# Kernel tuning notes

Hardware: AMD Instinct MI355X
Metric: run time of the kernel (lower is better)

Reference implementation:

```python
import jax, jax.numpy as jnp
import numpy as np

H = 1024

def gru_step(x, h, W_ih, W_hh, b_ih, b_hh):
    # torch.nn.GRUCell math; gate order r, z, n
    gi = x @ W_ih.T + b_ih            # [N, 3H]
    gh = h @ W_hh.T + b_hh            # [N, 3H]
    i_r, i_z, i_n = jnp.split(gi, 3, axis=-1)
    h_r, h_z, h_n = jnp.split(gh, 3, axis=-1)
    r = jax.nn.sigmoid(i_r + h_r)
    z = jax.nn.sigmoid(i_z + h_z)
    n = jnp.tanh(i_n + r * h_n)
    return (1.0 - z) * n + z * h


def setup_inputs() -> dict:
    key = jax.random.key(0)
    ks = jax.random.split(key, 12)
    V, Nr, Na = 256, 4096, 4096
    s = 1.0 / np.sqrt(H)
    return {
        'state': jax.random.normal(ks[0], (1, H), jnp.float32),
        'rel_tokens': jax.random.randint(ks[1], (Nr, 3), 0, V, jnp.int32),
        'attr_tokens': jax.random.randint(ks[2], (Na, 2), 0, V, jnp.int32),
        'table': jax.random.normal(ks[3], (V, H), jnp.float32),
        'W_emb': jax.random.normal(ks[4], (H, H), jnp.float32) * s,
        'b_emb': jnp.zeros((H,), jnp.float32),
        'W_ih': jax.random.normal(ks[5], (3 * H, H), jnp.float32) * s,
        'W_hh': jax.random.normal(ks[6], (3 * H, H), jnp.float32) * s,
        'b_ih': jnp.zeros((3 * H,), jnp.float32),
        'b_hh': jnp.zeros((3 * H,), jnp.float32),
        'W1': jax.random.normal(ks[7], (H, H), jnp.float32) * s,
        'b1': jnp.zeros((H,), jnp.float32),
        'W2': jax.random.normal(ks[8], (H, H), jnp.float32) * s,
        'b2': jnp.zeros((H,), jnp.float32),
        'W3': jax.random.normal(ks[9], (1, H), jnp.float32) * s,
        'b3': jnp.zeros((1,), jnp.float32),
        'eps': jax.random.uniform(ks[10], (1,), jnp.float32) * 0.1,
    }


def reference(state, rel_tokens, attr_tokens, table, W_emb, b_emb,
              W_ih, W_hh, b_ih, b_hh, W1, b1, W2, b2, W3, b3, eps):
    Nr, Na = rel_tokens.shape[0], attr_tokens.shape[0]
    # per-clause token embeddings passed through embedding_layer (Linear)
    rel_e = jnp.einsum('nte,he->nth', table[rel_tokens], W_emb) + b_emb   # [Nr,3,H]
    att_e = jnp.einsum('nte,he->nth', table[attr_tokens], W_emb) + b_emb  # [Na,2,H]

    # relation clauses: 3 chained GRU steps from global state
    h = jnp.broadcast_to(state, (Nr, H))
    for t in range(3):
        h = gru_step(rel_e[:, t], h, W_ih, W_hh, b_ih, b_hh)
    rel_h = h
    # attribute clauses: 2 chained GRU steps from global state
    h = jnp.broadcast_to(state, (Na, H))
    for t in range(2):
        h = gru_step(att_e[:, t], h, W_ih, W_hh, b_ih, b_hh)
    attr_h = h

    clause = jnp.concatenate([rel_h, attr_h], axis=0)          # [N, H]
    x = jax.nn.relu(clause @ W1.T + b1)
    x = jax.nn.relu(x @ W2.T + b2)
    logits = (x @ W3.T + b3).reshape(1, -1)                    # [1, N]
    probs = jax.nn.softmax(logits, axis=1)                     # softmax over clauses
    n = jnp.float32(probs.shape[1])
    probs = probs * (1.0 - eps[0]) + eps[0] / n                # eps smoothing
    return probs
```

## Files before the change

kernel.cpp:

```cpp
#include <hip/hip_runtime.h>
#include <math.h>

#define H 1024
#define H3 3072
#define NVOC 256

typedef __attribute__((ext_vector_type(8))) short bf16x8;
typedef __attribute__((ext_vector_type(4))) float f32x4;

__device__ __forceinline__ float sigf(float x) { return 1.0f / (1.0f + expf(-x)); }

__device__ __forceinline__ unsigned short f2bf(float f) {
    unsigned int u = __float_as_uint(f);
    u = (u + 0x7fffu + ((u >> 16) & 1u)) >> 16;
    return (unsigned short)u;
}
__device__ __forceinline__ float bf2f(unsigned short u) {
    return __uint_as_float(((unsigned int)u) << 16);
}

#define MM256(MH, AV, BV)                                                          \
    __builtin_amdgcn_s_setprio(1);                                                 \
    _Pragma("unroll")                                                              \
    for (int m_ = 0; m_ < 4; ++m_)                                                 \
        _Pragma("unroll")                                                          \
        for (int n_ = 0; n_ < 4; ++n_)                                             \
            acc[(MH) * 4 + m_][n_] = __builtin_amdgcn_mfma_f32_16x16x32_bf16(      \
                AV[m_], BV[n_], acc[(MH) * 4 + m_][n_], 0, 0, 0);                  \
    __builtin_amdgcn_s_setprio(0);

#define RDA256(BUF, MH, KQ)                                                        \
    _Pragma("unroll")                                                              \
    for (int m_ = 0; m_ < 4; ++m_)                                                 \
        a[m_] = *reinterpret_cast<const bf16x8*>(                                  \
            ldsb + (BUF) * 65536 + (g * 128 + (MH) * 64 + m_ * 16 + fr) * 128 +    \
            (((KQ) * 4 + fq) ^ (fr & 7)) * 16);

#define RDB256(BUF, KQ, DST)                                                       \
    _Pragma("unroll")                                                              \
    for (int n_ = 0; n_ < 4; ++n_)                                                 \
        DST[n_] = *reinterpret_cast<const bf16x8*>(                                \
            ldsb + (BUF) * 65536 + 32768 + (wn + n_ * 16 + fr) * 128 +             \
            (((KQ) * 4 + fq) ^ (fr & 7)) * 16);

#define BAR256() __builtin_amdgcn_s_barrier()

template<bool RELU, int OUT_MODE>
__global__ __launch_bounds__(512, 2)
void gemm256(const unsigned short* __restrict__ A, const unsigned short* __restrict__ W,
             const float* __restrict__ bias, void* __restrict__ C,
             int N, int K, int gx,
             const float* __restrict__ w3, float* __restrict__ logits)
{
    __shared__ unsigned short lds[65536];
    char* ldsb = (char*)lds;
    const int tid = threadIdx.x;
    const int wid = tid >> 6, lane = tid & 63;

    const int nwg = gridDim.x;
    const int cpx = nwg >> 3;
    const int bid = blockIdx.x;
    const int swz = (bid & 7) * cpx + (bid >> 3);
    const int bm = (swz / gx) * 256;
    const int bn = (swz % gx) * 256;

    const int g = wid >> 2;
    const int wn = (wid & 3) * 64;
    const int fr = lane & 15, fq = lane >> 4;

    const int sr = tid >> 3;
    const int sc = ((tid & 7) ^ (sr & 7)) * 8;
    auto stage_unit = [&](int t, int u) {
        const unsigned short* src = (u < 4)
            ? A + (size_t)(bm + u * 64 + sr) * K + t * 64 + sc
            : W + (size_t)(bn + (u - 4) * 64 + sr) * K + t * 64 + sc;
        char* dst = ldsb + (t & 1) * 65536 + u * 8192 + tid * 16;
        __builtin_amdgcn_global_load_lds(
            (const __attribute__((address_space(1))) void*)src,
            (__attribute__((address_space(3))) void*)dst, 16, 0, 0);
    };

    f32x4 acc[8][4];
#pragma unroll
    for (int i = 0; i < 8; i++)
#pragma unroll
        for (int j = 0; j < 4; j++) acc[i][j] = (f32x4){0.f, 0.f, 0.f, 0.f};
    bf16x8 a[4], b0[4], b1[4];

    const int nt = K >> 6;

#pragma unroll
    for (int u = 0; u < 8; ++u) stage_unit(0, u);
    stage_unit(1, 0); stage_unit(1, 2); stage_unit(1, 4);
    stage_unit(1, 5); stage_unit(1, 6); stage_unit(1, 7);
    asm volatile("s_waitcnt vmcnt(6)" ::: "memory");
    __builtin_amdgcn_sched_barrier(0);
    BAR256();

    for (int t = 0; t < nt; ++t) {
        const int buf = t & 1;
        RDB256(buf, 0, b0); RDA256(buf, 0, 0);
        if (t + 1 < nt) stage_unit(t + 1, 1);
        MM256(0, a, b0); BAR256();
        RDB256(buf, 1, b1); RDA256(buf, 0, 1);
        if (t + 1 < nt) stage_unit(t + 1, 3);
        MM256(0, a, b1); BAR256();
        RDA256(buf, 1, 0);
        if (t + 2 < nt) { stage_unit(t + 2, 0); stage_unit(t + 2, 2); stage_unit(t + 2, 4); }
        MM256(1, a, b0); BAR256();
        RDA256(buf, 1, 1);
        if (t + 2 < nt) { stage_unit(t + 2, 5); stage_unit(t + 2, 6); stage_unit(t + 2, 7); }
        MM256(1, a, b1);
        if (t + 2 < nt) {
            asm volatile("s_waitcnt vmcnt(6)" ::: "memory");
            __builtin_amdgcn_sched_barrier(0);
        } else if (t + 1 < nt) {
            asm volatile("s_waitcnt vmcnt(0)" ::: "memory");
            __builtin_amdgcn_sched_barrier(0);
        }
        BAR256();
    }

    if (OUT_MODE == 2) {
        float rs[8][4];
#pragma unroll
        for (int m = 0; m < 8; m++)
#pragma unroll
            for (int j = 0; j < 4; j++) rs[m][j] = 0.f;
#pragma unroll
        for (int n = 0; n < 4; n++) {
            const int col = bn + wn + n * 16 + fr;
            const float bv = bias[col];
            const float wv = w3[col];
#pragma unroll
            for (int m = 0; m < 8; m++)
#pragma unroll
                for (int j = 0; j < 4; j++) {
                    float v = acc[m][n][j] + bv;
                    if (RELU) v = fmaxf(v, 0.f);
                    rs[m][j] = fmaf(v, wv, rs[m][j]);
                }
        }
#pragma unroll
        for (int m = 0; m < 8; m++)
#pragma unroll
            for (int j = 0; j < 4; j++) {
                float s = rs[m][j];
                s += __shfl_xor(s, 1); s += __shfl_xor(s, 2);
                s += __shfl_xor(s, 4); s += __shfl_xor(s, 8);
                if (fr == 0) {
                    const int row = bm + g * 128 + (m >> 2) * 64 + (m & 3) * 16 + fq * 4 + j;
                    atomicAdd(logits + row, s);
                }
            }
    } else {
#pragma unroll
        for (int m = 0; m < 8; m++) {
#pragma unroll
            for (int n = 0; n < 4; n++) {
                const int col = bn + wn + n * 16 + fr;
                const float bv = bias[col];
#pragma unroll
                for (int j = 0; j < 4; j++) {
                    const int row = bm + g * 128 + (m >> 2) * 64 + (m & 3) * 16 + fq * 4 + j;
                    float v = acc[m][n][j] + bv;
                    if (RELU) v = fmaxf(v, 0.f);
                    ((unsigned short*)C)[(size_t)row * N + col] = f2bf(v);
                }
            }
        }
    }
}

template<bool RELU, int OUT_MODE>
__global__ __launch_bounds__(512, 2)
void gemm_n(const unsigned short* __restrict__ A, const unsigned short* __restrict__ W,
            const float* __restrict__ bias, void* __restrict__ C,
            int N, int K, int gx,
            const float* __restrict__ w3, float* __restrict__ logits)
{
    __shared__ unsigned short lds[73728];
    char* ldsb = (char*)lds;
    const int tid = threadIdx.x;
    const int wid = tid >> 6, lane = tid & 63;

    const int nwg = gridDim.x;
    const int cpx = nwg >> 3;
    const int bid = blockIdx.x;
    const int swz = (bid & 7) * cpx + (bid >> 3);
    const int bm = (swz / gx) * 128;
    const int bn = (swz % gx) * 256;

    const int g = wid >> 2;
    const int wn = (wid & 3) * 64;
    const int fr = lane & 15, fq = lane >> 4;

    const int sr = tid >> 3;
    const int sc = ((tid & 7) ^ (sr & 7)) * 8;
    auto stage_unit = [&](int t, int u) {
        const unsigned short* src = (u < 2)
            ? A + (size_t)(bm + u * 64 + sr) * K + t * 64 + sc
            : W + (size_t)(bn + (u - 2) * 64 + sr) * K + t * 64 + sc;
        char* dst = ldsb + (t % 3) * 49152 + u * 8192 + tid * 16;
        __builtin_amdgcn_global_load_lds(
            (const __attribute__((address_space(1))) void*)src,
            (__attribute__((address_space(3))) void*)dst, 16, 0, 0);
    };

    f32x4 acc[4][4];
#pragma unroll
    for (int i = 0; i < 4; i++)
#pragma unroll
        for (int j = 0; j < 4; j++) acc[i][j] = (f32x4){0.f, 0.f, 0.f, 0.f};
    bf16x8 a[4], b[4];

    const int nt = K >> 6;

#pragma unroll
    for (int u = 0; u < 6; ++u) stage_unit(0, u);
#pragma unroll
    for (int u = 0; u < 6; ++u) stage_unit(1, u);
    asm volatile("s_waitcnt vmcnt(6)" ::: "memory");
    __builtin_amdgcn_sched_barrier(0);
    __builtin_amdgcn_s_barrier();

    for (int t = 0; t < nt; ++t) {
        const int buf = (t % 3) * 49152;
#pragma unroll
        for (int n_ = 0; n_ < 4; ++n_)
            b[n_] = *reinterpret_cast<const bf16x8*>(
                ldsb + buf + 16384 + (wn + n_ * 16 + fr) * 128 + ((fq) ^ (fr & 7)) * 16);
#pragma unroll
        for (int m_ = 0; m_ < 4; ++m_)
            a[m_] = *reinterpret_cast<const bf16x8*>(
                ldsb + buf + (g * 64 + m_ * 16 + fr) * 128 + ((fq) ^ (fr & 7)) * 16);
        if (t + 2 < nt) { stage_unit(t + 2, 0); stage_unit(t + 2, 1); stage_unit(t + 2, 2); }
        __builtin_amdgcn_s_setprio(1);
#pragma unroll
        for (int m_ = 0; m_ < 4; ++m_)
#pragma unroll
            for (int n_ = 0; n_ < 4; ++n_)
                acc[m_][n_] = __builtin_amdgcn_mfma_f32_16x16x32_bf16(a[m_], b[n_], acc[m_][n_], 0, 0, 0);
        __builtin_amdgcn_s_setprio(0);
        __builtin_amdgcn_s_barrier();
#pragma unroll
        for (int n_ = 0; n_ < 4; ++n_)
            b[n_] = *reinterpret_cast<const bf16x8*>(
                ldsb + buf + 16384 + (wn + n_ * 16 + fr) * 128 + ((4 + fq) ^ (fr & 7)) * 16);
#pragma unroll
        for (int m_ = 0; m_ < 4; ++m_)
            a[m_] = *reinterpret_cast<const bf16x8*>(
                ldsb + buf + (g * 64 + m_ * 16 + fr) * 128 + ((4 + fq) ^ (fr & 7)) * 16);
        if (t + 2 < nt) { stage_unit(t + 2, 3); stage_unit(t + 2, 4); stage_unit(t + 2, 5); }
        __builtin_amdgcn_s_setprio(1);
#pragma unroll
        for (int m_ = 0; m_ < 4; ++m_)
#pragma unroll
            for (int n_ = 0; n_ < 4; ++n_)
                acc[m_][n_] = __builtin_amdgcn_mfma_f32_16x16x32_bf16(a[m_], b[n_], acc[m_][n_], 0, 0, 0);
        __builtin_amdgcn_s_setprio(0);
        if (t + 2 < nt) {
            asm volatile("s_waitcnt vmcnt(6)" ::: "memory");
            __builtin_amdgcn_sched_barrier(0);
        } else if (t + 1 < nt) {
            asm volatile("s_waitcnt vmcnt(0)" ::: "memory");
            __builtin_amdgcn_sched_barrier(0);
        }
        __builtin_amdgcn_s_barrier();
    }

    if (OUT_MODE == 2) {
        float rs[4][4];
#pragma unroll
        for (int m = 0; m < 4; m++)
#pragma unroll
            for (int j = 0; j < 4; j++) rs[m][j] = 0.f;
#pragma unroll
        for (int n = 0; n < 4; n++) {
            const int col = bn + wn + n * 16 + fr;
            const float bv = bias[col];
            const float wv = w3[col];
#pragma unroll
            for (int m = 0; m < 4; m++)
#pragma unroll
                for (int j = 0; j < 4; j++) {
                    float v = acc[m][n][j] + bv;
                    if (RELU) v = fmaxf(v, 0.f);
                    rs[m][j] = fmaf(v, wv, rs[m][j]);
                }
        }
#pragma unroll
        for (int m = 0; m < 4; m++)
#pragma unroll
            for (int j = 0; j < 4; j++) {
                float s = rs[m][j];
                s += __shfl_xor(s, 1); s += __shfl_xor(s, 2);
                s += __shfl_xor(s, 4); s += __shfl_xor(s, 8);
                if (fr == 0) atomicAdd(logits + bm + g * 64 + m * 16 + fq * 4 + j, s);
            }
    } else {
#pragma unroll
        for (int m = 0; m < 4; m++) {
#pragma unroll
            for (int n = 0; n < 4; n++) {
                const int col = bn + wn + n * 16 + fr;
                const float bv = bias[col];
#pragma unroll
                for (int j = 0; j < 4; j++) {
                    const int row = bm + g * 64 + m * 16 + fq * 4 + j;
                    float v = acc[m][n][j] + bv;
                    if (RELU) v = fmaxf(v, 0.f);
                    ((unsigned short*)C)[(size_t)row * N + col] = f2bf(v);
                }
            }
        }
    }
}

template<bool RELU, int OUT_MODE>
__global__ __launch_bounds__(256)
void gemm_bf16(const unsigned short* __restrict__ A, const unsigned short* __restrict__ W,
               const float* __restrict__ bias, void* __restrict__ C,
               int N, int K, int gx, int Kc,
               const float* __restrict__ w3, float* __restrict__ logits)
{
    __shared__ unsigned short As[4][128 * 32];
    __shared__ unsigned short Ws[4][128 * 32];
    const int tid = threadIdx.x;
    const int wid = tid >> 6, lane = tid & 63;

    const int nwg = gridDim.x;
    const int cpx = nwg >> 3;
    const int bid = blockIdx.x;
    const int swz = (bid & 7) * cpx + (bid >> 3);
    const int bm = (swz / gx) * 128;
    const int bn = (swz % gx) * 128;
    const int k_base = blockIdx.y * Kc;
    const int nt = Kc >> 5;

    const int wm = (wid >> 1) * 64, wn = (wid & 1) * 64;
    const int fr = lane & 15;
    const int fq = lane >> 4;
    const int perm = fq ^ (fr & 3);

    f32x4 acc[4][4];
#pragma unroll
    for (int i = 0; i < 4; i++)
#pragma unroll
        for (int j = 0; j < 4; j++) acc[i][j] = (f32x4){0.f, 0.f, 0.f, 0.f};

    const int srow = tid >> 2;
    const int schunk = (tid & 3) ^ (srow & 3);
    const unsigned short* aS = A + (size_t)(bm + srow) * K + k_base + schunk * 8;
    const unsigned short* wS = W + (size_t)(bn + srow) * K + k_base + schunk * 8;
    const size_t rstep = (size_t)64 * K;

    auto stage = [&](int b, int t) {
        const unsigned short* a0 = aS + t * 32;
        const unsigned short* w0 = wS + t * 32;
        __builtin_amdgcn_global_load_lds(
            (const __attribute__((address_space(1))) void*)a0,
            (__attribute__((address_space(3))) void*)(&As[b][wid * 512]), 16, 0, 0);
        __builtin_amdgcn_global_load_lds(
            (const __attribute__((address_space(1))) void*)(a0 + rstep),
            (__attribute__((address_space(3))) void*)(&As[b][2048 + wid * 512]), 16, 0, 0);
        __builtin_amdgcn_global_load_lds(
            (const __attribute__((address_space(1))) void*)w0,
            (__attribute__((address_space(3))) void*)(&Ws[b][wid * 512]), 16, 0, 0);
        __builtin_amdgcn_global_load_lds(
            (const __attribute__((address_space(1))) void*)(w0 + rstep),
            (__attribute__((address_space(3))) void*)(&Ws[b][2048 + wid * 512]), 16, 0, 0);
    };

    stage(0, 0);
    if (nt > 1) stage(1, 1);
    if (nt > 2) stage(2, 2);

    for (int t = 0; t < nt; ++t) {
        if (t + 2 < nt)      asm volatile("s_waitcnt vmcnt(8)" ::: "memory");
        else if (t + 1 < nt) asm volatile("s_waitcnt vmcnt(4)" ::: "memory");
        else                 asm volatile("s_waitcnt vmcnt(0)" ::: "memory");
        __builtin_amdgcn_s_barrier();
        __builtin_amdgcn_sched_barrier(0);
        if (t + 3 < nt) stage((t + 3) & 3, t + 3);

        const unsigned short* as = &As[t & 3][0];
        const unsigned short* ws = &Ws[t & 3][0];
        bf16x8 a[4], b[4];
#pragma unroll
        for (int m = 0; m < 4; m++)
            a[m] = *reinterpret_cast<const bf16x8*>(as + (wm + m * 16 + fr) * 32 + perm * 8);
#pragma unroll
        for (int n = 0; n < 4; n++)
            b[n] = *reinterpret_cast<const bf16x8*>(ws + (wn + n * 16 + fr) * 32 + perm * 8);
        __builtin_amdgcn_s_setprio(1);
#pragma unroll
        for (int m = 0; m < 4; m++)
#pragma unroll
            for (int n = 0; n < 4; n++)
                acc[m][n] = __builtin_amdgcn_mfma_f32_16x16x32_bf16(a[m], b[n], acc[m][n], 0, 0, 0);
        __builtin_amdgcn_s_setprio(0);
    }

    if (OUT_MODE == 3) {
        float* Cf = (float*)C;
#pragma unroll
        for (int m = 0; m < 4; m++)
#pragma unroll
            for (int n = 0; n < 4; n++) {
                const int col = bn + wn + n * 16 + fr;
#pragma unroll
                for (int j = 0; j < 4; j++) {
                    const int row = bm + wm + m * 16 + fq * 4 + j;
                    atomicAdd(Cf + (size_t)row * N + col, acc[m][n][j]);
                }
            }
    } else {
#pragma unroll
        for (int m = 0; m < 4; m++) {
#pragma unroll
            for (int n = 0; n < 4; n++) {
                const int col = bn + wn + n * 16 + fr;
                const float bv = bias[col];
#pragma unroll
                for (int j = 0; j < 4; j++) {
                    const int row = bm + wm + m * 16 + fq * 4 + j;
                    float v = acc[m][n][j] + bv;
                    if (RELU) v = fmaxf(v, 0.f);
                    if (OUT_MODE == 1)
                        ((unsigned short*)C)[(size_t)row * N + col] = f2bf(v);
                    else
                        ((float*)C)[(size_t)row * N + col] = v;
                }
            }
        }
    }
}

__global__ __launch_bounds__(256)
void prep(const float* __restrict__ W_hh, const float* __restrict__ W_ih,
          const float* __restrict__ W1, const float* __restrict__ W2,
          const float* __restrict__ W_emb, const float* __restrict__ table,
          const float* __restrict__ state, const float* __restrict__ b_emb,
          const float* __restrict__ b_ih, const float* __restrict__ b_hh,
          unsigned short* __restrict__ W_hhb, unsigned short* __restrict__ W_ihb,
          unsigned short* __restrict__ W1b, unsigned short* __restrict__ W2b,
          unsigned short* __restrict__ W_embb, unsigned short* __restrict__ tableb,
          float* __restrict__ gh0, float* __restrict__ emb32, float* __restrict__ Gi,
          float* __restrict__ gh1, float* __restrict__ logits)
{
    int b = blockIdx.x;
    const int t = threadIdx.x;
    if (b < 3072) {
        float4 w = *reinterpret_cast<const float4*>(W_hh + (size_t)b * H + t * 4);
        ushort4 o; o.x = f2bf(w.x); o.y = f2bf(w.y); o.z = f2bf(w.z); o.w = f2bf(w.w);
        *reinterpret_cast<ushort4*>(W_hhb + (size_t)b * H + t * 4) = o;
        float4 sv = *reinterpret_cast<const float4*>(state + t * 4);
        float s = w.x * sv.x + w.y * sv.y + w.z * sv.z + w.w * sv.w;
#pragma unroll
        for (int off = 32; off; off >>= 1) s += __shfl_down(s, off);
        __shared__ float ps[4];
        if ((t & 63) == 0) ps[t >> 6] = s;
        __syncthreads();
        if (t == 0) gh0[b] = ps[0] + ps[1] + ps[2] + ps[3] + b_hh[b];
        return;
    }
    b -= 3072;
    const float* src = nullptr; unsigned short* dst = nullptr;
    if (b < 3072)      { src = W_ih;  dst = W_ihb; }
    else if ((b -= 3072) < 1024) { src = W1; dst = W1b; }
    else if ((b -= 1024) < 1024) { src = W2; dst = W2b; }
    else if ((b -= 1024) < 1024) { src = W_emb; dst = W_embb; }
    else if ((b -= 1024) < 256)  { src = table; dst = tableb; }
    else {
        b -= 256;
        if (b < 256) {
            int i = b * 1024 + t * 4;
            *reinterpret_cast<float4*>(emb32 + i) =
                *reinterpret_cast<const float4*>(b_emb + (i & (H - 1)));
        } else if ((b -= 256) < 768) {
            int i = b * 1024 + t * 4;
            *reinterpret_cast<float4*>(Gi + i) =
                *reinterpret_cast<const float4*>(b_ih + i % H3);
        } else if ((b -= 768) < 768) {
            int i = b * 1024 + t * 4;
            *reinterpret_cast<float4*>(gh1 + i) =
                *reinterpret_cast<const float4*>(b_hh + i % H3);
        } else {
            b -= 768;
            int i = b * 1024 + t * 4;
            *reinterpret_cast<float4*>(logits + i) = (float4){0.f, 0.f, 0.f, 0.f};
        }
        return;
    }
    const int off = b * 1024 + t * 4;
    float4 v = *reinterpret_cast<const float4*>(src + off);
    ushort4 o; o.x = f2bf(v.x); o.y = f2bf(v.y); o.z = f2bf(v.z); o.w = f2bf(v.w);
    *reinterpret_cast<ushort4*>(dst + off) = o;
}

__global__ void cvt_emb(const float* __restrict__ in, unsigned short* __restrict__ out)
{
    int i = (blockIdx.x * blockDim.x + threadIdx.x) * 4;
    float4 v = *reinterpret_cast<const float4*>(in + i);
    ushort4 o;
    o.x = f2bf(v.x); o.y = f2bf(v.y); o.z = f2bf(v.z); o.w = f2bf(v.w);
    *reinterpret_cast<ushort4*>(out + i) = o;
}

__global__ void h1_combine(const float* __restrict__ Gi, const float* __restrict__ gh0,
                           const float* __restrict__ state, float* __restrict__ h1,
                           unsigned short* __restrict__ h1b)
{
    int idx = blockIdx.x * blockDim.x + threadIdx.x;
    int v = idx >> 10, h = idx & (H - 1);
    const float* g = Gi + (size_t)v * H3;
    float r = sigf(g[h] + gh0[h]);
    float z = sigf(g[H + h] + gh0[H + h]);
    float n = tanhf(fmaf(r, gh0[2 * H + h], g[2 * H + h]));
    float v2 = (1.f - z) * n + z * state[h];
    h1[idx] = v2;
    h1b[idx] = f2bf(v2);
}

__global__ void step2_both(const int* __restrict__ rel, const int* __restrict__ attr, int Nr,
                           const float* __restrict__ Gi, const float* __restrict__ gh1,
                           const float* __restrict__ h1,
                           unsigned short* __restrict__ h2b, unsigned short* __restrict__ attr_out)
{
    int idx = blockIdx.x * blockDim.x + threadIdx.x;
    int row = idx >> 10, h = idx & (H - 1);
    int t0, t1, orow = row;
    unsigned short* dst;
    if (row < Nr) { t0 = rel[row * 3 + 0]; t1 = rel[row * 3 + 1]; dst = h2b; }
    else { orow = row - Nr; t0 = attr[orow * 2 + 0]; t1 = attr[orow * 2 + 1]; dst = attr_out; }
    const float* g = Gi + (size_t)t1 * H3;
    const float* gh = gh1 + (size_t)t0 * H3;
    float r = sigf(g[h] + gh[h]);
    float z = sigf(g[H + h] + gh[H + h]);
    float n = tanhf(fmaf(r, gh[2 * H + h], g[2 * H + h]));
    float v = (1.f - z) * n + z * h1[(size_t)t0 * H + h];
    dst[(size_t)orow * H + h] = f2bf(v);
}

__global__ void step3_rel(const int* __restrict__ toks,
                          const float* __restrict__ Gi, const unsigned short* __restrict__ gh2b,
                          const unsigned short* __restrict__ h2b, unsigned short* __restrict__ outb)
{
    int idx = blockIdx.x * blockDim.x + threadIdx.x;
    int row = idx >> 10, h = idx & (H - 1);
    int t2 = toks[row * 3 + 2];
    const float* g = Gi + (size_t)t2 * H3;
    const unsigned short* gh = gh2b + (size_t)row * H3;
    float r = sigf(g[h] + bf2f(gh[h]));
    float z = sigf(g[H + h] + bf2f(gh[H + h]));
    float n = tanhf(fmaf(r, bf2f(gh[2 * H + h]), g[2 * H + h]));
    outb[idx] = f2bf((1.f - z) * n + z * bf2f(h2b[idx]));
}

__global__ void softmax_eps(const float* __restrict__ logits, const float* __restrict__ epsp,
                            float* __restrict__ out, int N)
{
    __shared__ float smax[16], ssum[16];
    int tid = threadIdx.x;
    int nw = blockDim.x >> 6;
    float m = -INFINITY;
    for (int i = tid; i < N; i += blockDim.x) m = fmaxf(m, logits[i]);
#pragma unroll
    for (int off = 32; off; off >>= 1) m = fmaxf(m, __shfl_down(m, off));
    if ((tid & 63) == 0) smax[tid >> 6] = m;
    __syncthreads();
    float M = smax[0];
    for (int i = 1; i < nw; i++) M = fmaxf(M, smax[i]);
    float s = 0.f;
    for (int i = tid; i < N; i += blockDim.x) s += expf(logits[i] - M);
#pragma unroll
    for (int off = 32; off; off >>= 1) s += __shfl_down(s, off);
    if ((tid & 63) == 0) ssum[tid >> 6] = s;
    __syncthreads();
    float S = 0.f;
    for (int i = 0; i < nw; i++) S += ssum[i];
    float e = epsp[0];
    float mul = (1.f - e) / S;
    float add = e / (float)N;
    for (int i = tid; i < N; i += blockDim.x) out[i] = expf(logits[i] - M) * mul + add;
}

extern "C" void kernel_launch(void* const* d_in, const int* in_sizes, int n_in,
                              void* d_out, int out_size, void* d_ws, size_t ws_size,
                              hipStream_t stream)
{
    const float* state       = (const float*)d_in[0];
    const int*   rel_tokens  = (const int*)d_in[1];
    const int*   attr_tokens = (const int*)d_in[2];
    const float* table       = (const float*)d_in[3];
    const float* W_emb       = (const float*)d_in[4];
    const float* b_emb       = (const float*)d_in[5];
    const float* W_ih        = (const float*)d_in[6];
    const float* W_hh        = (const float*)d_in[7];
    const float* b_ih        = (const float*)d_in[8];
    const float* b_hh        = (const float*)d_in[9];
    const float* W1          = (const float*)d_in[10];
    const float* b1          = (const float*)d_in[11];
    const float* W2          = (const float*)d_in[12];
    const float* b2          = (const float*)d_in[13];
    const float* W3          = (const float*)d_in[14];
    const float* eps         = (const float*)d_in[16];

    const int Nr = in_sizes[1] / 3;
    const int Na = in_sizes[2] / 2;
    const int Ntot = Nr + Na;

    float* ws     = (float*)d_ws;
    float* Gi     = ws;
    float* gh0    = Gi + NVOC * H3;
    float* h1     = gh0 + H3;
    float* gh1    = h1 + NVOC * H;
    float* emb32  = gh1 + NVOC * H3;
    float* logits = emb32 + NVOC * H;
    unsigned short* W_hhb   = (unsigned short*)(logits + Ntot);
    unsigned short* W_ihb   = W_hhb + (size_t)H3 * H;
    unsigned short* W1b     = W_ihb + (size_t)H3 * H;
    unsigned short* W2b     = W1b + (size_t)H * H;
    unsigned short* W_embb  = W2b + (size_t)H * H;
    unsigned short* tableb  = W_embb + (size_t)H * H;
    unsigned short* embb    = tableb + (size_t)NVOC * H;
    unsigned short* h1b     = embb + (size_t)NVOC * H;
    unsigned short* h2b     = h1b + (size_t)NVOC * H;
    unsigned short* gh2b    = h2b + (size_t)Nr * H;
    unsigned short* clauseb = gh2b + (size_t)Nr * H3;
    unsigned short* x1b     = clauseb + (size_t)Ntot * H;

    prep<<<11272, 256, 0, stream>>>(W_hh, W_ih, W1, W2, W_emb, table, state,
                                    b_emb, b_ih, b_hh,
                                    W_hhb, W_ihb, W1b, W2b, W_embb, tableb,
                                    gh0, emb32, Gi, gh1, logits);

    gemm_bf16<false, 3><<<dim3((H / 128) * (NVOC / 128), 4), 256, 0, stream>>>(
        tableb, W_embb, nullptr, emb32, H, H, H / 128, H / 4, nullptr, nullptr);
    cvt_emb<<<NVOC * H / 4 / 256, 256, 0, stream>>>(emb32, embb);
    gemm_bf16<false, 3><<<dim3((H3 / 128) * (NVOC / 128), 4), 256, 0, stream>>>(
        embb, W_ihb, nullptr, Gi, H3, H, H3 / 128, H / 4, nullptr, nullptr);
    h1_combine<<<NVOC * H / 256, 256, 0, stream>>>(Gi, gh0, state, h1, h1b);
    gemm_bf16<false, 3><<<dim3((H3 / 128) * (NVOC / 128), 4), 256, 0, stream>>>(
        h1b, W_hhb, nullptr, gh1, H3, H, H3 / 128, H / 4, nullptr, nullptr);
    step2_both<<<Ntot * (H / 256), 256, 0, stream>>>(rel_tokens, attr_tokens, Nr,
                                                     Gi, gh1, h1, h2b,
                                                     clauseb + (size_t)Nr * H);
    gemm256<false, 1><<<(Nr / 256) * (H3 / 256), 512, 0, stream>>>(
        h2b, W_hhb, b_hh, gh2b, H3, H, H3 / 256, nullptr, nullptr);
    step3_rel<<<Nr * (H / 256), 256, 0, stream>>>(rel_tokens, Gi, gh2b, h2b, clauseb);
    gemm_n<true, 1><<<(Ntot / 128) * (H / 256), 512, 0, stream>>>(
        clauseb, W1b, b1, x1b, H, H, H / 256, nullptr, nullptr);
    gemm_n<true, 2><<<(Ntot / 128) * (H / 256), 512, 0, stream>>>(
        x1b, W2b, b2, nullptr, H, H, H / 256, W3, logits);
    softmax_eps<<<1, 1024, 0, stream>>>(logits, eps, (float*)d_out, Ntot);
}
```

Measured before the change: 282.0 us.

## Fuse step-3 GRU gate math into the recurrent GEMM epilogue

Measured after the change: 282.2 us. Within noise of the previous version (+0.1%).

```diff
diff --git a/kernel.cpp b/kernel.cpp
--- a/kernel.cpp
+++ b/kernel.cpp
@@ -19,41 +19,13 @@
     return __uint_as_float(((unsigned int)u) << 16);
 }
 
-#define MM256(MH, AV, BV)                                                          \
-    __builtin_amdgcn_s_setprio(1);                                                 \
-    _Pragma("unroll")                                                              \
-    for (int m_ = 0; m_ < 4; ++m_)                                                 \
-        _Pragma("unroll")                                                          \
-        for (int n_ = 0; n_ < 4; ++n_)                                             \
-            acc[(MH) * 4 + m_][n_] = __builtin_amdgcn_mfma_f32_16x16x32_bf16(      \
-                AV[m_], BV[n_], acc[(MH) * 4 + m_][n_], 0, 0, 0);                  \
-    __builtin_amdgcn_s_setprio(0);
-
-#define RDA256(BUF, MH, KQ)                                                        \
-    _Pragma("unroll")                                                              \
-    for (int m_ = 0; m_ < 4; ++m_)                                                 \
-        a[m_] = *reinterpret_cast<const bf16x8*>(                                  \
-            ldsb + (BUF) * 65536 + (g * 128 + (MH) * 64 + m_ * 16 + fr) * 128 +    \
-            (((KQ) * 4 + fq) ^ (fr & 7)) * 16);
-
-#define RDB256(BUF, KQ, DST)                                                       \
-    _Pragma("unroll")                                                              \
-    for (int n_ = 0; n_ < 4; ++n_)                                                 \
-        DST[n_] = *reinterpret_cast<const bf16x8*>(                                \
-            ldsb + (BUF) * 65536 + 32768 + (wn + n_ * 16 + fr) * 128 +             \
-            (((KQ) * 4 + fq) ^ (fr & 7)) * 16);
-
-#define BAR256() __builtin_amdgcn_s_barrier()
-
-template<bool RELU, int OUT_MODE>
 __global__ __launch_bounds__(512, 2)
-void gemm256(const unsigned short* __restrict__ A, const unsigned short* __restrict__ W,
-             const float* __restrict__ bias, void* __restrict__ C,
-             int N, int K, int gx,
-             const float* __restrict__ w3, float* __restrict__ logits)
-{
-    __shared__ unsigned short lds[65536];
-    char* ldsb = (char*)lds;
+void gemm_gru(const unsigned short* __restrict__ A, const unsigned short* __restrict__ W,
+              const float* __restrict__ bias, const float* __restrict__ Gi,
+              const int* __restrict__ toks, unsigned short* __restrict__ outb,
+              int K, int gx)
+{
+    __shared__ char ldsb[114688];
     const int tid = threadIdx.x;
     const int wid = tid >> 6, lane = tid & 63;
 
@@ -62,10 +34,10 @@
     const int bid = blockIdx.x;
     const int swz = (bid & 7) * cpx + (bid >> 3);
     const int bm = (swz / gx) * 256;
-    const int bn = (swz % gx) * 256;
-
-    const int g = wid >> 2;
-    const int wn = (wid & 3) * 64;
+    const int hbase = (swz % gx) * 64;
+
+    const int gm = wid >> 2;
+    const int hb = (wid & 3) * 16;
     const int fr = lane & 15, fq = lane >> 4;
 
     const int sr = tid >> 3;
@@ -73,101 +45,97 @@
     auto stage_unit = [&](int t, int u) {
         const unsigned short* src = (u < 4)
             ? A + (size_t)(bm + u * 64 + sr) * K + t * 64 + sc
-            : W + (size_t)(bn + (u - 4) * 64 + sr) * K + t * 64 + sc;
-        char* dst = ldsb + (t & 1) * 65536 + u * 8192 + tid * 16;
+            : W + (size_t)((u - 4) * 1024 + hbase + sr) * K + t * 64 + sc;
+        char* dst = ldsb + (t & 1) * 57344 + ((u < 4) ? u * 8192 : 32768 + (u - 4) * 8192)
+                    + tid * 16;
         __builtin_amdgcn_global_load_lds(
             (const __attribute__((address_space(1))) void*)src,
             (__attribute__((address_space(3))) void*)dst, 16, 0, 0);
     };
 
-    f32x4 acc[8][4];
+    f32x4 acc[8][3];
 #pragma unroll
     for (int i = 0; i < 8; i++)
 #pragma unroll
-        for (int j = 0; j < 4; j++) acc[i][j] = (f32x4){0.f, 0.f, 0.f, 0.f};
-    bf16x8 a[4], b0[4], b1[4];
+        for (int j = 0; j < 3; j++) acc[i][j] = (f32x4){0.f, 0.f, 0.f, 0.f};
+    bf16x8 a[4], b0[3], b1[3];
 
     const int nt = K >> 6;
 
 #pragma unroll
-    for (int u = 0; u < 8; ++u) stage_unit(0, u);
-    stage_unit(1, 0); stage_unit(1, 2); stage_unit(1, 4);
-    stage_unit(1, 5); stage_unit(1, 6); stage_unit(1, 7);
-    asm volatile("s_waitcnt vmcnt(6)" ::: "memory");
+    for (int u = 0; u < 7; ++u) stage_unit(0, u);
+    stage_unit(1, 0); stage_unit(1, 2);
+    stage_unit(1, 4); stage_unit(1, 5); stage_unit(1, 6);
+    asm volatile("s_waitcnt vmcnt(5)" ::: "memory");
     __builtin_amdgcn_sched_barrier(0);
-    BAR256();
+    __builtin_amdgcn_s_barrier();
+
+#define RDA_G(BUF, MH, KQ)                                                         \
+    _Pragma("unroll")                                                              \
+    for (int m_ = 0; m_ < 4; ++m_)                                                 \
+        a[m_] = *reinterpret_cast<const bf16x8*>(                                  \
+            ldsb + (BUF) * 57344 + (gm * 128 + (MH) * 64 + m_ * 16 + fr) * 128 +   \
+            (((KQ) * 4 + fq) ^ (fr & 7)) * 16);
+#define RDB_G(BUF, KQ, DST)                                                        \
+    _Pragma("unroll")                                                              \
+    for (int n_ = 0; n_ < 3; ++n_)                                                 \
+        DST[n_] = *reinterpret_cast<const bf16x8*>(                                \
+            ldsb + (BUF) * 57344 + 32768 + (n_ * 64 + hb + fr) * 128 +             \
+            (((KQ) * 4 + fq) ^ (fr & 7)) * 16);
+#define MM_G(MH, BV)                                                               \
+    __builtin_amdgcn_s_setprio(1);                                                 \
+    _Pragma("unroll")                                                              \
+    for (int m_ = 0; m_ < 4; ++m_)                                                 \
+        _Pragma("unroll")                                                          \
+        for (int n_ = 0; n_ < 3; ++n_)                                             \
+            acc[(MH) * 4 + m_][n_] = __builtin_amdgcn_mfma_f32_16x16x32_bf16(      \
+                a[m_], BV[n_], acc[(MH) * 4 + m_][n_], 0, 0, 0);                   \
+    __builtin_amdgcn_s_setprio(0);
 
     for (int t = 0; t < nt; ++t) {
         const int buf = t & 1;
-        RDB256(buf, 0, b0); RDA256(buf, 0, 0);
+        RDB_G(buf, 0, b0); RDA_G(buf, 0, 0);
         if (t + 1 < nt) stage_unit(t + 1, 1);
-        MM256(0, a, b0); BAR256();
-        RDB256(buf, 1, b1); RDA256(buf, 0, 1);
+        MM_G(0, b0); __builtin_amdgcn_s_barrier();
+        RDB_G(buf, 1, b1); RDA_G(buf, 0, 1);
         if (t + 1 < nt) stage_unit(t + 1, 3);
-        MM256(0, a, b1); BAR256();
-        RDA256(buf, 1, 0);
-        if (t + 2 < nt) { stage_unit(t + 2, 0); stage_unit(t + 2, 2); stage_unit(t + 2, 4); }
-        MM256(1, a, b0); BAR256();
-        RDA256(buf, 1, 1);
-        if (t + 2 < nt) { stage_unit(t + 2, 5); stage_unit(t + 2, 6); stage_unit(t + 2, 7); }
-        MM256(1, a, b1);
+        MM_G(0, b1); __builtin_amdgcn_s_barrier();
+        RDA_G(buf, 1, 0);
+        if (t + 2 < nt) { stage_unit(t + 2, 0); stage_unit(t + 2, 2); }
+        MM_G(1, b0); __builtin_amdgcn_s_barrier();
+        RDA_G(buf, 1, 1);
+        if (t + 2 < nt) { stage_unit(t + 2, 4); stage_unit(t + 2, 5); stage_unit(t + 2, 6); }
+        MM_G(1, b1);
         if (t + 2 < nt) {
-            asm volatile("s_waitcnt vmcnt(6)" ::: "memory");
+            asm volatile("s_waitcnt vmcnt(5)" ::: "memory");
             __builtin_amdgcn_sched_barrier(0);
         } else if (t + 1 < nt) {
             asm volatile("s_waitcnt vmcnt(0)" ::: "memory");
             __builtin_amdgcn_sched_barrier(0);
         }
-        BAR256();
-    }
-
-    if (OUT_MODE == 2) {
-        float rs[8][4];
-#pragma unroll
-        for (int m = 0; m < 8; m++)
-#pragma unroll
-            for (int j = 0; j < 4; j++) rs[m][j] = 0.f;
-#pragma unroll
-        for (int n = 0; n < 4; n++) {
-            const int col = bn + wn + n * 16 + fr;
-            const float bv = bias[col];
-            const float wv = w3[col];
-#pragma unroll
-            for (int m = 0; m < 8; m++)
-#pragma unroll
-                for (int j = 0; j < 4; j++) {
-                    float v = acc[m][n][j] + bv;
-                    if (RELU) v = fmaxf(v, 0.f);
-                    rs[m][j] = fmaf(v, wv, rs[m][j]);
-                }
-        }
-#pragma unroll
-        for (int m = 0; m < 8; m++)
-#pragma unroll
-            for (int j = 0; j < 4; j++) {
-                float s = rs[m][j];
-                s += __shfl_xor(s, 1); s += __shfl_xor(s, 2);
-                s += __shfl_xor(s, 4); s += __shfl_xor(s, 8);
-                if (fr == 0) {
-                    const int row = bm + g * 128 + (m >> 2) * 64 + (m & 3) * 16 + fq * 4 + j;
-                    atomicAdd(logits + row, s);
-                }
-            }
-    } else {
-#pragma unroll
-        for (int m = 0; m < 8; m++) {
-#pragma unroll
-            for (int n = 0; n < 4; n++) {
-                const int col = bn + wn + n * 16 + fr;
-                const float bv = bias[col];
-#pragma unroll
-                for (int j = 0; j < 4; j++) {
-                    const int row = bm + g * 128 + (m >> 2) * 64 + (m & 3) * 16 + fq * 4 + j;
-                    float v = acc[m][n][j] + bv;
-                    if (RELU) v = fmaxf(v, 0.f);
-                    ((unsigned short*)C)[(size_t)row * N + col] = f2bf(v);
-                }
-            }
+        __builtin_amdgcn_s_barrier();
+    }
+#undef RDA_G
+#undef RDB_G
+#undef MM_G
+
+    const int h = hbase + hb + fr;
+    const float br = bias[h], bz = bias[1024 + h], bn = bias[2048 + h];
+#pragma unroll
+    for (int mi = 0; mi < 8; ++mi) {
+#pragma unroll
+        for (int jj = 0; jj < 4; ++jj) {
+            const int row = bm + gm * 128 + (mi >> 2) * 64 + (mi & 3) * 16 + fq * 4 + jj;
+            const int t2 = toks[row * 3 + 2];
+            const float* gi = Gi + (size_t)t2 * H3;
+            const float gh2r = acc[mi][0][jj] + br;
+            const float gh2z = acc[mi][1][jj] + bz;
+            const float gh2n = acc[mi][2][jj] + bn;
+            const float r = sigf(gi[h] + gh2r);
+            const float z = sigf(gi[1024 + h] + gh2z);
+            const float n = tanhf(fmaf(r, gh2n, gi[2048 + h]));
+            const float hv = bf2f(A[(size_t)row * 1024 + h]);
+            outb[(size_t)row * 1024 + h] = f2bf((1.f - z) * n + z * hv);
         }
     }
 }
@@ -543,21 +511,6 @@
     dst[(size_t)orow * H + h] = f2bf(v);
 }
 
-__global__ void step3_rel(const int* __restrict__ toks,
-                          const float* __restrict__ Gi, const unsigned short* __restrict__ gh2b,
-                          const unsigned short* __restrict__ h2b, unsigned short* __restrict__ outb)
-{
-    int idx = blockIdx.x * blockDim.x + threadIdx.x;
-    int row = idx >> 10, h = idx & (H - 1);
-    int t2 = toks[row * 3 + 2];
-    const float* g = Gi + (size_t)t2 * H3;
-    const unsigned short* gh = gh2b + (size_t)row * H3;
-    float r = sigf(g[h] + bf2f(gh[h]));
-    float z = sigf(g[H + h] + bf2f(gh[H + h]));
-    float n = tanhf(fmaf(r, bf2f(gh[2 * H + h]), g[2 * H + h]));
-    outb[idx] = f2bf((1.f - z) * n + z * bf2f(h2b[idx]));
-}
-
 __global__ void softmax_eps(const float* __restrict__ logits, const float* __restrict__ epsp,
                             float* __restrict__ out, int N)
 {
@@ -627,8 +580,7 @@
     unsigned short* embb    = tableb + (size_t)NVOC * H;
     unsigned short* h1b     = embb + (size_t)NVOC * H;
     unsigned short* h2b     = h1b + (size_t)NVOC * H;
-    unsigned short* gh2b    = h2b + (size_t)Nr * H;
-    unsigned short* clauseb = gh2b + (size_t)Nr * H3;
+    unsigned short* clauseb = h2b + (size_t)Nr * H;
     unsigned short* x1b     = clauseb + (size_t)Ntot * H;
 
     prep<<<11272, 256, 0, stream>>>(W_hh, W_ih, W1, W2, W_emb, table, state,
@@ -647,9 +599,8 @@
     step2_both<<<Ntot * (H / 256), 256, 0, stream>>>(rel_tokens, attr_tokens, Nr,
                                                      Gi, gh1, h1, h2b,
                                                      clauseb + (size_t)Nr * H);
-    gemm256<false, 1><<<(Nr / 256) * (H3 / 256), 512, 0, stream>>>(
-        h2b, W_hhb, b_hh, gh2b, H3, H, H3 / 256, nullptr, nullptr);
-    step3_rel<<<Nr * (H / 256), 256, 0, stream>>>(rel_tokens, Gi, gh2b, h2b, clauseb);
+    gemm_gru<<<16 * 16, 512, 0, stream>>>(h2b, W_hhb, b_hh, Gi, rel_tokens,
+                                          clauseb, H, H / 64);
     gemm_n<true, 1><<<(Ntot / 128) * (H / 256), 512, 0, stream>>>(
         clauseb, W1b, b1, x1b, H, H, H / 256, nullptr, nullptr);
     gemm_n<true, 2><<<(Ntot / 128) * (H / 256), 512, 0, stream>>>(
```
